# Kernel optimization log

Hardware: AMD Instinct MI355X
Metric: run time of the kernel (lower is better)

## Reference

```python
import jax, jax.numpy as jnp
import numpy as np


def setup_inputs() -> dict:
    key = jax.random.key(0)
    kx, ks = jax.random.split(key)
    M, N, D = 8192, 8192, 512
    X = jax.random.normal(kx, (M, D), dtype=jnp.float32)
    svs = jax.random.normal(ks, (N, D), dtype=jnp.float32)
    # scale = 1/(2*sigma^2); a plausible fitted value for standard-normal data
    scale = jnp.asarray(0.01, dtype=jnp.float32)
    return {"X": X, "svs": svs, "scale": scale}


def reference(X, svs, scale):
    N, D = svs.shape
    x2 = jnp.sum(X * X, axis=-1, keepdims=True)          # [M, 1]
    s2 = jnp.sum(svs * svs, axis=-1)                      # [N]
    dist2 = x2 + s2[None, :] - 2.0 * (X @ svs.T)          # [M, N]
    dist2 = jnp.maximum(dist2, 0.0)
    log_p = (jax.scipy.special.logsumexp(-scale * dist2, axis=-1)
             - jnp.log(jnp.asarray(N, dtype=X.dtype))
             + (D / 2) * jnp.log(scale / jnp.pi))
    return log_p
```

## Files before the change

kernel.cpp:

```cpp
#include <hip/hip_runtime.h>
#include <hip/hip_bf16.h>
#include <hip/hip_fp8.h>
#include <math.h>

typedef __attribute__((ext_vector_type(4))) int   int4v;
typedef __attribute__((ext_vector_type(8))) int   int8v;
typedef __attribute__((ext_vector_type(4))) float f32x4;

#define AS1 __attribute__((address_space(1)))
#define AS3 __attribute__((address_space(3)))

__global__ __launch_bounds__(256) void prep_kernel(
    const float* __restrict__ X, const float* __restrict__ S,
    unsigned char* __restrict__ Xq, unsigned char* __restrict__ Sq,
    float* __restrict__ x2, float* __restrict__ s2,
    float* __restrict__ rowsum, int M, int R, int Dv)
{
    const int gid  = blockIdx.x * 256 + threadIdx.x;
    const int nthr = gridDim.x * 256;

    for (int i = gid; i < M; i += nthr) rowsum[i] = 0.f;

    const int lane = threadIdx.x & 63;
    const int wid  = gid >> 6;
    const int nw   = nthr >> 6;

    for (int row = wid; row < R; row += nw) {
        const float* rp;
        unsigned char* op;
        float* sq;
        if (row < M) { rp = X + (size_t)row * Dv;       op = Xq + (size_t)row * Dv;       sq = x2 + row; }
        else         { rp = S + (size_t)(row - M) * Dv; op = Sq + (size_t)(row - M) * Dv; sq = s2 + (row - M); }

        float acc = 0.f;
        for (int k = lane * 8; k < Dv; k += 64 * 8) {
            float4 v0 = *(const float4*)(rp + k);
            float4 v1 = *(const float4*)(rp + k + 4);
            acc += v0.x * v0.x + v0.y * v0.y + v0.z * v0.z + v0.w * v0.w;
            acc += v1.x * v1.x + v1.y * v1.y + v1.z * v1.z + v1.w * v1.w;
            union { __hip_fp8_e4m3 h[8]; uint2 u; } pk;
            pk.h[0] = __hip_fp8_e4m3(v0.x);
            pk.h[1] = __hip_fp8_e4m3(v0.y);
            pk.h[2] = __hip_fp8_e4m3(v0.z);
            pk.h[3] = __hip_fp8_e4m3(v0.w);
            pk.h[4] = __hip_fp8_e4m3(v1.x);
            pk.h[5] = __hip_fp8_e4m3(v1.y);
            pk.h[6] = __hip_fp8_e4m3(v1.z);
            pk.h[7] = __hip_fp8_e4m3(v1.w);
            *(uint2*)(op + k) = pk.u;
        }
#pragma unroll
        for (int off = 1; off < 64; off <<= 1)
            acc += __shfl_xor(acc, off, 64);
        if (lane == 0) *sq = acc;
    }
}

__global__ __launch_bounds__(256, 2) void kde_gemm512(
    const unsigned char* __restrict__ Xq,
    const unsigned char* __restrict__ Sq,
    const float* __restrict__ x2,
    const float* __restrict__ s2,
    const float* __restrict__ scale_p,
    float* __restrict__ rowsum,
    int M, int N)
{
    __shared__ char smem[65536];
    unsigned char* Bs = (unsigned char*)smem;

    const int tid  = threadIdx.x;
    const int wave = tid >> 6;
    const int lane = tid & 63;
    const int quad = lane >> 4;
    const int l16  = lane & 15;

    const int m0 = blockIdx.x * 128;
    const int n0 = blockIdx.y * 128;

    const float sc = *scale_p;

    const int srow = tid >> 5;
    const int cg   = (tid & 31) ^ srow;
    const unsigned char* gB = Sq + (size_t)(n0 + srow) * 512 + cg * 16;
#pragma unroll
    for (int r = 0; r < 16; ++r)
        __builtin_amdgcn_global_load_lds(
            (const AS1 void*)(gB + (size_t)r * 8 * 512),
            (AS3 void*)(smem + r * 4096 + wave * 1024),
            16, 0, 0);

    int8v af[2][4];
    const unsigned char* gA = Xq + (size_t)(m0 + wave * 32 + l16) * 512 + quad * 32;
#pragma unroll
    for (int mi = 0; mi < 2; ++mi)
#pragma unroll
        for (int c = 0; c < 4; ++c) {
            int4v lo = *(const int4v*)(gA + mi * 16 * 512 + c * 128);
            int4v hi = *(const int4v*)(gA + mi * 16 * 512 + c * 128 + 16);
            af[mi][c] = (int8v){lo.x, lo.y, lo.z, lo.w, hi.x, hi.y, hi.z, hi.w};
        }

    f32x4 acc[2][8] = {};

    __syncthreads();

    const int e = l16 & 7;
#pragma unroll
    for (int c = 0; c < 4; ++c) {
#pragma unroll
        for (int ni = 0; ni < 8; ++ni) {
            const unsigned char* rowp = Bs + (size_t)(ni * 16 + l16) * 512;
            int4v lo = *(const int4v*)(rowp + (8 * c + ((2 * quad)     ^ e)) * 16);
            int4v hi = *(const int4v*)(rowp + (8 * c + ((2 * quad + 1) ^ e)) * 16);
            int8v bf = (int8v){lo.x, lo.y, lo.z, lo.w, hi.x, hi.y, hi.z, hi.w};
            acc[0][ni] = __builtin_amdgcn_mfma_scale_f32_16x16x128_f8f6f4(
                af[0][c], bf, acc[0][ni], 0, 0, 0, 0x7F7F7F7F, 0, 0x7F7F7F7F);
            acc[1][ni] = __builtin_amdgcn_mfma_scale_f32_16x16x128_f8f6f4(
                af[1][c], bf, acc[1][ni], 0, 0, 0, 0x7F7F7F7F, 0, 0x7F7F7F7F);
        }
    }

    __syncthreads();
    float* wred = (float*)smem + wave * (32 * 20);

    float s2v[8];
#pragma unroll
    for (int ni = 0; ni < 8; ++ni)
        s2v[ni] = s2[n0 + ni * 16 + l16];

#pragma unroll
    for (int mi = 0; mi < 2; ++mi) {
#pragma unroll
        for (int r = 0; r < 4; ++r) {
            const int rl = mi * 16 + quad * 4 + r;
            const float xv = x2[m0 + wave * 32 + rl];
            float sum = 0.f;
#pragma unroll
            for (int ni = 0; ni < 8; ++ni) {
                float d2 = xv + s2v[ni] - 2.0f * acc[mi][ni][r];
                d2 = fmaxf(d2, 0.f);
                sum += __expf(-sc * d2);
            }
            wred[rl * 20 + l16] = sum;
        }
    }
    __syncthreads();

    if (lane < 32) {
        float* rp = wred + lane * 20;
        float4 p0 = *(float4*)(rp + 0);
        float4 p1 = *(float4*)(rp + 4);
        float4 p2 = *(float4*)(rp + 8);
        float4 p3 = *(float4*)(rp + 12);
        float s = (p0.x + p0.y + p0.z + p0.w) + (p1.x + p1.y + p1.z + p1.w)
                + (p2.x + p2.y + p2.z + p2.w) + (p3.x + p3.y + p3.z + p3.w);
        atomicAdd(&rowsum[m0 + wave * 32 + lane], s);
    }
}

__global__ __launch_bounds__(256, 3) void kde_gemm_generic(
    const unsigned char* __restrict__ Xq, const unsigned char* __restrict__ Sq,
    const float* __restrict__ x2, const float* __restrict__ s2,
    const float* __restrict__ scale_p, float* __restrict__ rowsum,
    int M, int N, int Dv)
{
    const int D = Dv;
    __shared__ char smem[32768];
    unsigned char* As = (unsigned char*)smem;
    unsigned char* Bs = (unsigned char*)(smem + 16384);

    const int tid  = threadIdx.x;
    const int wave = tid >> 6;
    const int lane = tid & 63;
    const int quad = lane >> 4;
    const int l16  = lane & 15;

    const int m0 = blockIdx.x * 128;
    const int n0 = blockIdx.y * 128;
    const int wm = (wave & 1) * 64;
    const int wn = (wave >> 1) * 64;

    const float sc = *scale_p;
    f32x4 acc[4][4] = {};

    const int srow0 = wave * 8 + (lane >> 3);
    const int cg    = (lane & 7) ^ (lane >> 3);
    const unsigned char* gA = Xq + (size_t)(m0 + srow0) * D + cg * 16;
    const unsigned char* gB = Sq + (size_t)(n0 + srow0) * D + cg * 16;

    for (int k0 = 0; k0 < D; k0 += 128) {
        __syncthreads();
#pragma unroll
        for (int rd = 0; rd < 4; ++rd)
            __builtin_amdgcn_global_load_lds(
                (const AS1 void*)(gA + (size_t)rd * 32 * D + k0),
                (AS3 void*)(smem + rd * 4096 + wave * 1024), 16, 0, 0);
#pragma unroll
        for (int rd = 0; rd < 4; ++rd)
            __builtin_amdgcn_global_load_lds(
                (const AS1 void*)(gB + (size_t)rd * 32 * D + k0),
                (AS3 void*)(smem + 16384 + rd * 4096 + wave * 1024), 16, 0, 0);
        __syncthreads();

        const int e = l16 & 7;
        int8v a_frag[4], b_frag[4];
#pragma unroll
        for (int mi = 0; mi < 4; ++mi) {
            const unsigned char* rowp = As + (wm + mi * 16 + l16) * 128;
            int4v lo = *(const int4v*)(rowp + ((2 * quad)     ^ e) * 16);
            int4v hi = *(const int4v*)(rowp + ((2 * quad + 1) ^ e) * 16);
            a_frag[mi] = (int8v){lo.x, lo.y, lo.z, lo.w, hi.x, hi.y, hi.z, hi.w};
        }
#pragma unroll
        for (int ni = 0; ni < 4; ++ni) {
            const unsigned char* rowp = Bs + (wn + ni * 16 + l16) * 128;
            int4v lo = *(const int4v*)(rowp + ((2 * quad)     ^ e) * 16);
            int4v hi = *(const int4v*)(rowp + ((2 * quad + 1) ^ e) * 16);
            b_frag[ni] = (int8v){lo.x, lo.y, lo.z, lo.w, hi.x, hi.y, hi.z, hi.w};
        }
#pragma unroll
        for (int mi = 0; mi < 4; ++mi)
#pragma unroll
            for (int ni = 0; ni < 4; ++ni)
                acc[mi][ni] = __builtin_amdgcn_mfma_scale_f32_16x16x128_f8f6f4(
                    a_frag[mi], b_frag[ni], acc[mi][ni],
                    0, 0, 0, 0x7F7F7F7F, 0, 0x7F7F7F7F);
    }

    __syncthreads();
    float* wred = (float*)smem + wave * (64 * 20);

    float s2v[4];
#pragma unroll
    for (int ni = 0; ni < 4; ++ni)
        s2v[ni] = s2[n0 + wn + ni * 16 + l16];

#pragma unroll
    for (int mi = 0; mi < 4; ++mi) {
#pragma unroll
        for (int r = 0; r < 4; ++r) {
            const int rowL = mi * 16 + quad * 4 + r;
            const float xv = x2[m0 + wm + rowL];
            float sum = 0.f;
#pragma unroll
            for (int ni = 0; ni < 4; ++ni) {
                float d2 = xv + s2v[ni] - 2.0f * acc[mi][ni][r];
                d2 = fmaxf(d2, 0.f);
                sum += __expf(-sc * d2);
            }
            wred[rowL * 20 + l16] = sum;
        }
    }
    __syncthreads();

    float4 p0 = *(float4*)(wred + lane * 20 + 0);
    float4 p1 = *(float4*)(wred + lane * 20 + 4);
    float4 p2 = *(float4*)(wred + lane * 20 + 8);
    float4 p3 = *(float4*)(wred + lane * 20 + 12);
    float s = (p0.x + p0.y + p0.z + p0.w) + (p1.x + p1.y + p1.z + p1.w)
            + (p2.x + p2.y + p2.z + p2.w) + (p3.x + p3.y + p3.z + p3.w);
    atomicAdd(&rowsum[m0 + wm + lane], s);
}

__global__ void finalize_kernel(const float* __restrict__ rowsum,
                                const float* __restrict__ scale_p,
                                float* __restrict__ out, int M, int N, int Dv) {
    const int m = blockIdx.x * 256 + threadIdx.x;
    if (m < M) {
        const float sc = *scale_p;
        const float cst = -logf((float)N) + 0.5f * (float)Dv * logf(sc / 3.14159265358979f);
        out[m] = logf(rowsum[m]) + cst;
    }
}

extern "C" void kernel_launch(void* const* d_in, const int* in_sizes, int n_in,
                              void* d_out, int out_size, void* d_ws, size_t ws_size,
                              hipStream_t stream) {
    const float* X       = (const float*)d_in[0];
    const float* S       = (const float*)d_in[1];
    const float* scale_p = (const float*)d_in[2];
    float* out = (float*)d_out;

    const int M  = out_size;
    const int Dv = in_sizes[0] / M;
    const int N  = in_sizes[1] / Dv;

    char* ws = (char*)d_ws;
    unsigned char* Xq = (unsigned char*)ws;
    unsigned char* Sq = (unsigned char*)(ws + (size_t)M * Dv);
    float* x2     = (float*)(ws + (size_t)M * Dv + (size_t)N * Dv);
    float* s2     = x2 + M;
    float* rowsum = s2 + N;

    prep_kernel<<<512, 256, 0, stream>>>(X, S, Xq, Sq, x2, s2, rowsum, M, M + N, Dv);

    dim3 grid(M / 128, N / 128);
    if (Dv == 512)
        kde_gemm512<<<grid, 256, 0, stream>>>(Xq, Sq, x2, s2, scale_p, rowsum, M, N);
    else
        kde_gemm_generic<<<grid, 256, 0, stream>>>(Xq, Sq, x2, s2, scale_p, rowsum, M, N, Dv);

    finalize_kernel<<<(M + 255) / 256, 256, 0, stream>>>(rowsum, scale_p, out, M, N, Dv);
}
```

Baseline: 141.7 us.

## Use 2x2 wave tiling with double-buffered K-chunks in FP8 KDE GEMM

Restructures the 128x128 FP8 GEMM tile so each wave computes a 64x64 sub-tile (2x2 wave grid) instead of 32x128. Both A and B are streamed through LDS in 128-wide K chunks with double buffering via global_load_lds, so the next chunk's load overlaps the current chunk's MFMAs. Previously the whole B tile was loaded at once and A went straight to registers. The change lowers LDS reads per MFMA (4+4 fragments feed 16 MFMAs) and cuts the up-front load latency. In exchange it adds a barrier per K step, and the epilogue now issues twice as many atomic adds per row because each row is split across two waves.

```diff
diff --git a/kernel.cpp b/kernel.cpp
--- a/kernel.cpp
+++ b/kernel.cpp
@@ -66,7 +66,6 @@
     int M, int N)
 {
     __shared__ char smem[65536];
-    unsigned char* Bs = (unsigned char*)smem;
 
     const int tid  = threadIdx.x;
     const int wave = tid >> 6;
@@ -76,86 +75,110 @@
 
     const int m0 = blockIdx.x * 128;
     const int n0 = blockIdx.y * 128;
+    const int wm = (wave & 1) * 64;
+    const int wn = (wave >> 1) * 64;
 
     const float sc = *scale_p;
 
-    const int srow = tid >> 5;
-    const int cg   = (tid & 31) ^ srow;
-    const unsigned char* gB = Sq + (size_t)(n0 + srow) * 512 + cg * 16;
-#pragma unroll
-    for (int r = 0; r < 16; ++r)
+    f32x4 acc[4][4] = {};
+
+    const int srow0 = wave * 8 + (lane >> 3);
+    const int cg    = (lane & 7) ^ (lane >> 3);
+    const unsigned char* gA = Xq + (size_t)(m0 + srow0) * 512 + cg * 16;
+    const unsigned char* gB = Sq + (size_t)(n0 + srow0) * 512 + cg * 16;
+
+#pragma unroll
+    for (int rd = 0; rd < 4; ++rd)
         __builtin_amdgcn_global_load_lds(
-            (const AS1 void*)(gB + (size_t)r * 8 * 512),
-            (AS3 void*)(smem + r * 4096 + wave * 1024),
-            16, 0, 0);
-
-    int8v af[2][4];
-    const unsigned char* gA = Xq + (size_t)(m0 + wave * 32 + l16) * 512 + quad * 32;
-#pragma unroll
-    for (int mi = 0; mi < 2; ++mi)
-#pragma unroll
-        for (int c = 0; c < 4; ++c) {
-            int4v lo = *(const int4v*)(gA + mi * 16 * 512 + c * 128);
-            int4v hi = *(const int4v*)(gA + mi * 16 * 512 + c * 128 + 16);
-            af[mi][c] = (int8v){lo.x, lo.y, lo.z, lo.w, hi.x, hi.y, hi.z, hi.w};
-        }
-
-    f32x4 acc[2][8] = {};
+            (const AS1 void*)(gA + (size_t)rd * 32 * 512),
+            (AS3 void*)(smem + rd * 4096 + wave * 1024), 16, 0, 0);
+#pragma unroll
+    for (int rd = 0; rd < 4; ++rd)
+        __builtin_amdgcn_global_load_lds(
+            (const AS1 void*)(gB + (size_t)rd * 32 * 512),
+            (AS3 void*)(smem + 16384 + rd * 4096 + wave * 1024), 16, 0, 0);
+
+    const int e = l16 & 7;
+
+#pragma unroll
+    for (int k = 0; k < 4; ++k) {
+        __syncthreads();
+
+        if (k < 3) {
+            const int k1 = (k + 1) * 128;
+            char* dst = smem + ((k + 1) & 1) * 32768;
+#pragma unroll
+            for (int rd = 0; rd < 4; ++rd)
+                __builtin_amdgcn_global_load_lds(
+                    (const AS1 void*)(gA + (size_t)rd * 32 * 512 + k1),
+                    (AS3 void*)(dst + rd * 4096 + wave * 1024), 16, 0, 0);
+#pragma unroll
+            for (int rd = 0; rd < 4; ++rd)
+                __builtin_amdgcn_global_load_lds(
+                    (const AS1 void*)(gB + (size_t)rd * 32 * 512 + k1),
+                    (AS3 void*)(dst + 16384 + rd * 4096 + wave * 1024), 16, 0, 0);
+        }
+
+        const unsigned char* As = (const unsigned char*)(smem + (k & 1) * 32768);
+        const unsigned char* Bs = As + 16384;
+
+        int8v a_frag[4], b_frag[4];
+#pragma unroll
+        for (int mi = 0; mi < 4; ++mi) {
+            const unsigned char* rowp = As + (wm + mi * 16 + l16) * 128;
+            int4v lo = *(const int4v*)(rowp + ((2 * quad)     ^ e) * 16);
+            int4v hi = *(const int4v*)(rowp + ((2 * quad + 1) ^ e) * 16);
+            a_frag[mi] = (int8v){lo.x, lo.y, lo.z, lo.w, hi.x, hi.y, hi.z, hi.w};
+        }
+#pragma unroll
+        for (int ni = 0; ni < 4; ++ni) {
+            const unsigned char* rowp = Bs + (wn + ni * 16 + l16) * 128;
+            int4v lo = *(const int4v*)(rowp + ((2 * quad)     ^ e) * 16);
+            int4v hi = *(const int4v*)(rowp + ((2 * quad + 1) ^ e) * 16);
+            b_frag[ni] = (int8v){lo.x, lo.y, lo.z, lo.w, hi.x, hi.y, hi.z, hi.w};
+        }
+#pragma unroll
+        for (int mi = 0; mi < 4; ++mi)
+#pragma unroll
+            for (int ni = 0; ni < 4; ++ni)
+                acc[mi][ni] = __builtin_amdgcn_mfma_scale_f32_16x16x128_f8f6f4(
+                    a_frag[mi], b_frag[ni], acc[mi][ni],
+                    0, 0, 0, 0x7F7F7F7F, 0, 0x7F7F7F7F);
+    }
 
     __syncthreads();
-
-    const int e = l16 & 7;
-#pragma unroll
-    for (int c = 0; c < 4; ++c) {
-#pragma unroll
-        for (int ni = 0; ni < 8; ++ni) {
-            const unsigned char* rowp = Bs + (size_t)(ni * 16 + l16) * 512;
-            int4v lo = *(const int4v*)(rowp + (8 * c + ((2 * quad)     ^ e)) * 16);
-            int4v hi = *(const int4v*)(rowp + (8 * c + ((2 * quad + 1) ^ e)) * 16);
-            int8v bf = (int8v){lo.x, lo.y, lo.z, lo.w, hi.x, hi.y, hi.z, hi.w};
-            acc[0][ni] = __builtin_amdgcn_mfma_scale_f32_16x16x128_f8f6f4(
-                af[0][c], bf, acc[0][ni], 0, 0, 0, 0x7F7F7F7F, 0, 0x7F7F7F7F);
-            acc[1][ni] = __builtin_amdgcn_mfma_scale_f32_16x16x128_f8f6f4(
-                af[1][c], bf, acc[1][ni], 0, 0, 0, 0x7F7F7F7F, 0, 0x7F7F7F7F);
-        }
-    }
-
-    __syncthreads();
-    float* wred = (float*)smem + wave * (32 * 20);
-
-    float s2v[8];
-#pragma unroll
-    for (int ni = 0; ni < 8; ++ni)
-        s2v[ni] = s2[n0 + ni * 16 + l16];
-
-#pragma unroll
-    for (int mi = 0; mi < 2; ++mi) {
+    float* wred = (float*)smem + wave * (64 * 20);
+
+    float s2v[4];
+#pragma unroll
+    for (int ni = 0; ni < 4; ++ni)
+        s2v[ni] = s2[n0 + wn + ni * 16 + l16];
+
+#pragma unroll
+    for (int mi = 0; mi < 4; ++mi) {
 #pragma unroll
         for (int r = 0; r < 4; ++r) {
-            const int rl = mi * 16 + quad * 4 + r;
-            const float xv = x2[m0 + wave * 32 + rl];
+            const int rowL = mi * 16 + quad * 4 + r;
+            const float xv = x2[m0 + wm + rowL];
             float sum = 0.f;
 #pragma unroll
-            for (int ni = 0; ni < 8; ++ni) {
+            for (int ni = 0; ni < 4; ++ni) {
                 float d2 = xv + s2v[ni] - 2.0f * acc[mi][ni][r];
                 d2 = fmaxf(d2, 0.f);
                 sum += __expf(-sc * d2);
             }
-            wred[rl * 20 + l16] = sum;
+            wred[rowL * 20 + l16] = sum;
         }
     }
     __syncthreads();
 
-    if (lane < 32) {
-        float* rp = wred + lane * 20;
-        float4 p0 = *(float4*)(rp + 0);
-        float4 p1 = *(float4*)(rp + 4);
-        float4 p2 = *(float4*)(rp + 8);
-        float4 p3 = *(float4*)(rp + 12);
-        float s = (p0.x + p0.y + p0.z + p0.w) + (p1.x + p1.y + p1.z + p1.w)
-                + (p2.x + p2.y + p2.z + p2.w) + (p3.x + p3.y + p3.z + p3.w);
-        atomicAdd(&rowsum[m0 + wave * 32 + lane], s);
-    }
+    float4 p0 = *(float4*)(wred + lane * 20 + 0);
+    float4 p1 = *(float4*)(wred + lane * 20 + 4);
+    float4 p2 = *(float4*)(wred + lane * 20 + 8);
+    float4 p3 = *(float4*)(wred + lane * 20 + 12);
+    float s = (p0.x + p0.y + p0.z + p0.w) + (p1.x + p1.y + p1.z + p1.w)
+            + (p2.x + p2.y + p2.z + p2.w) + (p3.x + p3.y + p3.z + p3.w);
+    atomicAdd(&rowsum[m0 + wm + lane], s);
 }
 
 __global__ __launch_bounds__(256, 3) void kde_gemm_generic(
```

After: 123.5 us. 12.8% less time.
